# Kernel tuning notes

Hardware: AMD Instinct MI355X
Metric: run time of the kernel (lower is better)

The kernel has to match this reference:

```python
import jax, jax.numpy as jnp
import numpy as np
from jax import lax

B = 32768        # batch
L = 1024         # input_size
K = 5            # kernel_size
PAD = K - 1      # circular padding = 4
FEA = L + (PAD - K // 2) * 2   # mem_fea_dim = 1028
MEM_DIM = 50
DATE_DIM = 32
SHRINK = 0.0025
EPS = 1e-12
DN = ('NCH', 'OIH', 'NCH')


def setup_inputs() -> dict:
    key = jax.random.key(0)
    ks = jax.random.split(key, 10)
    s = 0.05
    return {
        'x': jax.random.normal(ks[0], (B, L), jnp.float32),
        'date_vector': jax.random.normal(ks[1], (B, DATE_DIM), jnp.float32),
        'conv_w': jax.random.normal(ks[2], (1, 1, K), jnp.float32) * s,    # Conv1d weight [out,in,k]
        'convt_w': jax.random.normal(ks[3], (1, 1, K), jnp.float32) * s,   # ConvTranspose1d weight
        'mem_W': jax.random.normal(ks[4], (MEM_DIM, FEA), jnp.float32) * s,      # memory bank (codebook)
        'date_W': jax.random.normal(ks[5], (MEM_DIM, DATE_DIM), jnp.float32) * s, # date addressing weights
        'fcw_w': jax.random.normal(ks[6], (1, L), jnp.float32) * s,
        'fcw_b': jnp.zeros((1,), jnp.float32),
        'fcb_w': jax.random.normal(ks[7], (1, L), jnp.float32) * s,
        'fcb_b': jnp.zeros((1,), jnp.float32),
    }


def _forward(x, date_vector, conv_w, convt_w, mem_W, date_W, fcw_w, fcw_b, fcb_w, fcb_b):
    # --- encode: 1-channel circular conv (bias forced to 0 in original forward) ---
    st = x[:, None, :]                                            # [B,1,L]
    stp = jnp.pad(st, ((0, 0), (0, 0), (PAD, PAD)), mode='wrap')  # circular pad
    st = lax.conv_general_dilated(stp, conv_w, (1,), 'VALID', dimension_numbers=DN)  # [B,1,FEA]

    # --- DateMemoryUnit: date-addressed read with hard shrink + L1 renorm ---
    scores = date_vector @ date_W.T                               # [B,MEM_DIM]
    att = jax.nn.softmax(scores, axis=-1)
    att = jax.nn.relu(att - SHRINK) * att / (jnp.abs(att - SHRINK) + EPS)
    att = att / (jnp.sum(jnp.abs(att), axis=-1, keepdims=True) + EPS)
    st_mem = att @ mem_W                                          # [B,FEA]
    st = st_mem.reshape(B, 1, FEA)

    # --- decode: ConvTranspose1d(k=5, stride=1, padding=4) == VALID conv with flipped kernel ---
    st = lax.conv_general_dilated(st, jnp.flip(convt_w, -1), (1,), 'VALID', dimension_numbers=DN)
    st = st[:, 0, :]                                              # [B,L]

    # --- trend blend ---
    mtf = 0.5
    weight = jnp.tanh(x @ fcw_w.T + fcw_b) * mtf + 1.0            # [B,1]
    bias = jnp.tanh(x @ fcb_w.T + fcb_b) * mtf                    # [B,1]
    st = st * weight + bias
    return st, weight, bias


def reference(x, date_vector, conv_w, convt_w, mem_W, date_W, fcw_w, fcw_b, fcb_w, fcb_b):
    return _forward(x, date_vector, conv_w, convt_w, mem_W, date_W, fcw_w, fcw_b, fcb_w, fcb_b)
```

## Files before the change

kernel.cpp:

```cpp
#include <hip/hip_runtime.h>
#include <hip/hip_bf16.h>

#define BB   32768
#define LL   1024
#define FEA  1028
#define MEM  50
#define DATE 32

typedef float  f32x4  __attribute__((ext_vector_type(4)));
typedef __bf16 bf16x8 __attribute__((ext_vector_type(8)));

__device__ __forceinline__ float wave_max(float v) {
    #pragma unroll
    for (int off = 32; off; off >>= 1) v = fmaxf(v, __shfl_xor(v, off));
    return v;
}
__device__ __forceinline__ float wave_sum(float v) {
    #pragma unroll
    for (int off = 32; off; off >>= 1) v += __shfl_xor(v, off);
    return v;
}

__global__ void prep_wc(const float* __restrict__ convt_w,
                        const float* __restrict__ mem_W,
                        __bf16* __restrict__ wc) {
    int idx = blockIdx.x * 256 + threadIdx.x;
    int n = idx >> 6, k = idx & 63;
    float acc = 0.f;
    if (k < MEM) {
        #pragma unroll
        for (int j = 0; j < 5; ++j)
            acc += convt_w[j] * mem_W[k * FEA + n + 4 - j];
    }
    wc[n * 64 + k] = (__bf16)acc;
}

__global__ __launch_bounds__(256) void memconv_fused(
        const float* __restrict__ x,
        const float* __restrict__ dv,
        const float* __restrict__ dW,
        const float* __restrict__ fcw_w, const float* __restrict__ fcw_b,
        const float* __restrict__ fcb_w, const float* __restrict__ fcb_b,
        const __bf16* __restrict__ wc,
        float* __restrict__ out) {
    __shared__ __bf16 att_s[16 * 80];
    __shared__ float  w_s[16], b_s[16];

    const int lane = threadIdx.x & 63;
    const int wid  = threadIdx.x >> 6;
    const int cg   = lane & 15;
    const int kg   = lane >> 4;
    const int b0   = blockIdx.x * 16;

    {
        int m = lane < MEM ? lane : MEM - 1;
        float dwv[DATE];
        const f32x4* dwp = (const f32x4*)(dW + m * DATE);
        #pragma unroll
        for (int c = 0; c < 8; ++c) {
            f32x4 v = dwp[c];
            #pragma unroll
            for (int j = 0; j < 4; ++j) dwv[c * 4 + j] = v[j];
        }
        #pragma unroll
        for (int rr = 0; rr < 4; ++rr) {
            int r = wid * 4 + rr;
            int b = b0 + r;
            const f32x4* dvp = (const f32x4*)(dv + (size_t)b * DATE);
            float sc = 0.f;
            #pragma unroll
            for (int c = 0; c < 8; ++c) {
                f32x4 v = dvp[c];
                #pragma unroll
                for (int j = 0; j < 4; ++j) sc += v[j] * dwv[c * 4 + j];
            }
            float scm = (lane < MEM) ? sc : -1e30f;
            float mx  = wave_max(scm);
            float e   = (lane < MEM) ? __expf(sc - mx) : 0.f;
            float s   = wave_sum(e);
            float p   = e / s;
            float d   = p - 0.0025f;
            float p2  = (d > 0.f) ? p * d / (d + 1e-12f) : 0.f;
            float s2  = wave_sum(p2) + 1e-12f;
            float att = p2 / s2;
            att_s[r * 80 + lane] = (lane < MEM) ? (__bf16)att : (__bf16)0.f;
        }
    }

    {
        int r = wid * 4 + kg;
        int b = b0 + r;
        float aw = 0.f, ab = 0.f;
        #pragma unroll
        for (int c = 0; c < 16; ++c) {
            int off = c * 64 + cg * 4;
            f32x4 xv = *(const f32x4*)(x + (size_t)b * LL + off);
            f32x4 wv = *(const f32x4*)(fcw_w + off);
            f32x4 bv = *(const f32x4*)(fcb_w + off);
            #pragma unroll
            for (int j = 0; j < 4; ++j) {
                aw += xv[j] * wv[j];
                ab += xv[j] * bv[j];
            }
        }
        #pragma unroll
        for (int off = 1; off <= 8; off <<= 1) {
            aw += __shfl_xor(aw, off);
            ab += __shfl_xor(ab, off);
        }
        if (cg == 0) {
            float w  = tanhf(aw + fcw_b[0]) * 0.5f + 1.0f;
            float bi = tanhf(ab + fcb_b[0]) * 0.5f;
            w_s[r] = w; b_s[r] = bi;
            out[(size_t)BB * LL + b]      = w;
            out[(size_t)BB * LL + BB + b] = bi;
        }
    }
    __syncthreads();

    {
        bf16x8 bfr0 = *(const bf16x8*)(att_s + cg * 80 + kg * 8);
        bf16x8 bfr1 = *(const bf16x8*)(att_s + cg * 80 + 32 + kg * 8);
        float wreg = w_s[cg], breg = b_s[cg];
        float* orow = out + (size_t)(b0 + cg) * LL + wid * 256 + kg * 4;
        const __bf16* wbase = wc + (wid * 256 + cg) * 64 + kg * 8;
        #pragma unroll
        for (int nt = 0; nt < 16; ++nt) {
            bf16x8 a0 = *(const bf16x8*)(wbase + nt * 16 * 64);
            bf16x8 a1 = *(const bf16x8*)(wbase + nt * 16 * 64 + 32);
            f32x4 acc = {0.f, 0.f, 0.f, 0.f};
            acc = __builtin_amdgcn_mfma_f32_16x16x32_bf16(a0, bfr0, acc, 0, 0, 0);
            acc = __builtin_amdgcn_mfma_f32_16x16x32_bf16(a1, bfr1, acc, 0, 0, 0);
            f32x4 v;
            #pragma unroll
            for (int r4 = 0; r4 < 4; ++r4)
                v[r4] = acc[r4] * wreg + breg;
            *(f32x4*)(orow + nt * 16) = v;
        }
    }
}

extern "C" void kernel_launch(void* const* d_in, const int* in_sizes, int n_in,
                              void* d_out, int out_size, void* d_ws, size_t ws_size,
                              hipStream_t stream) {
    const float* x     = (const float*)d_in[0];
    const float* dv    = (const float*)d_in[1];
    const float* convt = (const float*)d_in[3];
    const float* memW  = (const float*)d_in[4];
    const float* dateW = (const float*)d_in[5];
    const float* fcww  = (const float*)d_in[6];
    const float* fcwb  = (const float*)d_in[7];
    const float* fcbw  = (const float*)d_in[8];
    const float* fcbb  = (const float*)d_in[9];
    float* out = (float*)d_out;
    __bf16* wc = (__bf16*)d_ws;

    prep_wc      <<<256,     256, 0, stream>>>(convt, memW, wc);
    memconv_fused<<<BB / 16, 256, 0, stream>>>(x, dv, dateW, fcww, fcwb, fcbw, fcbb, wc, out);
}
```

Before: 285.7 us.

## Stage MFMA output through LDS for coalesced row stores; restructure trend reduction

The MFMA results are written into a per-wave LDS staging tile and then read back so that each store instruction writes 256 contiguous bytes of an output row. Previously each lane wrote 16-byte pieces scattered across 16 rows. The fc trend dot products now read x with full-wave contiguous float4 loads, four rows per wave, and reduce across the whole wave. This adds LDS traffic and about 18KB of shared memory per block, which may lower occupancy.

```diff
diff --git a/kernel.cpp b/kernel.cpp
--- a/kernel.cpp
+++ b/kernel.cpp
@@ -43,8 +43,9 @@
         const float* __restrict__ fcb_w, const float* __restrict__ fcb_b,
         const __bf16* __restrict__ wc,
         float* __restrict__ out) {
-    __shared__ __bf16 att_s[16 * 80];
+    __shared__ __bf16 att_s[16 * 72];
     __shared__ float  w_s[16], b_s[16];
+    __shared__ float  stage[4][16 * 72];
 
     const int lane = threadIdx.x & 63;
     const int wid  = threadIdx.x >> 6;
@@ -65,8 +66,7 @@
         #pragma unroll
         for (int rr = 0; rr < 4; ++rr) {
             int r = wid * 4 + rr;
-            int b = b0 + r;
-            const f32x4* dvp = (const f32x4*)(dv + (size_t)b * DATE);
+            const f32x4* dvp = (const f32x4*)(dv + (size_t)(b0 + r) * DATE);
             float sc = 0.f;
             #pragma unroll
             for (int c = 0; c < 8; ++c) {
@@ -83,59 +83,79 @@
             float p2  = (d > 0.f) ? p * d / (d + 1e-12f) : 0.f;
             float s2  = wave_sum(p2) + 1e-12f;
             float att = p2 / s2;
-            att_s[r * 80 + lane] = (lane < MEM) ? (__bf16)att : (__bf16)0.f;
+            att_s[r * 72 + lane] = (lane < MEM) ? (__bf16)att : (__bf16)0.f;
         }
     }
 
     {
-        int r = wid * 4 + kg;
-        int b = b0 + r;
-        float aw = 0.f, ab = 0.f;
+        f32x4 wv[4], bv[4];
         #pragma unroll
-        for (int c = 0; c < 16; ++c) {
-            int off = c * 64 + cg * 4;
-            f32x4 xv = *(const f32x4*)(x + (size_t)b * LL + off);
-            f32x4 wv = *(const f32x4*)(fcw_w + off);
-            f32x4 bv = *(const f32x4*)(fcb_w + off);
+        for (int c = 0; c < 4; ++c) {
+            wv[c] = *(const f32x4*)(fcw_w + c * 256 + lane * 4);
+            bv[c] = *(const f32x4*)(fcb_w + c * 256 + lane * 4);
+        }
+        f32x4 xv[4][4];
+        #pragma unroll
+        for (int rr = 0; rr < 4; ++rr)
             #pragma unroll
-            for (int j = 0; j < 4; ++j) {
-                aw += xv[j] * wv[j];
-                ab += xv[j] * bv[j];
+            for (int c = 0; c < 4; ++c)
+                xv[rr][c] = *(const f32x4*)(x + (size_t)(b0 + wid * 4 + rr) * LL
+                                              + c * 256 + lane * 4);
+        #pragma unroll
+        for (int rr = 0; rr < 4; ++rr) {
+            int r = wid * 4 + rr;
+            float aw = 0.f, ab = 0.f;
+            #pragma unroll
+            for (int c = 0; c < 4; ++c)
+                #pragma unroll
+                for (int j = 0; j < 4; ++j) {
+                    aw += xv[rr][c][j] * wv[c][j];
+                    ab += xv[rr][c][j] * bv[c][j];
+                }
+            #pragma unroll
+            for (int off = 1; off <= 32; off <<= 1) {
+                aw += __shfl_xor(aw, off);
+                ab += __shfl_xor(ab, off);
             }
-        }
-        #pragma unroll
-        for (int off = 1; off <= 8; off <<= 1) {
-            aw += __shfl_xor(aw, off);
-            ab += __shfl_xor(ab, off);
-        }
-        if (cg == 0) {
             float w  = tanhf(aw + fcw_b[0]) * 0.5f + 1.0f;
             float bi = tanhf(ab + fcb_b[0]) * 0.5f;
-            w_s[r] = w; b_s[r] = bi;
-            out[(size_t)BB * LL + b]      = w;
-            out[(size_t)BB * LL + BB + b] = bi;
+            if (lane == 0) {
+                w_s[r] = w; b_s[r] = bi;
+                out[(size_t)BB * LL + (b0 + r)]      = w;
+                out[(size_t)BB * LL + BB + (b0 + r)] = bi;
+            }
         }
     }
     __syncthreads();
 
     {
-        bf16x8 bfr0 = *(const bf16x8*)(att_s + cg * 80 + kg * 8);
-        bf16x8 bfr1 = *(const bf16x8*)(att_s + cg * 80 + 32 + kg * 8);
-        float wreg = w_s[cg], breg = b_s[cg];
-        float* orow = out + (size_t)(b0 + cg) * LL + wid * 256 + kg * 4;
-        const __bf16* wbase = wc + (wid * 256 + cg) * 64 + kg * 8;
+        bf16x8 bfr0 = *(const bf16x8*)(att_s + cg * 72 + kg * 8);
+        bf16x8 bfr1 = *(const bf16x8*)(att_s + cg * 72 + 32 + kg * 8);
+        float* st = stage[wid];
+        const int n0 = wid * 256;
         #pragma unroll
-        for (int nt = 0; nt < 16; ++nt) {
-            bf16x8 a0 = *(const bf16x8*)(wbase + nt * 16 * 64);
-            bf16x8 a1 = *(const bf16x8*)(wbase + nt * 16 * 64 + 32);
-            f32x4 acc = {0.f, 0.f, 0.f, 0.f};
-            acc = __builtin_amdgcn_mfma_f32_16x16x32_bf16(a0, bfr0, acc, 0, 0, 0);
-            acc = __builtin_amdgcn_mfma_f32_16x16x32_bf16(a1, bfr1, acc, 0, 0, 0);
-            f32x4 v;
+        for (int R = 0; R < 4; ++R) {
             #pragma unroll
-            for (int r4 = 0; r4 < 4; ++r4)
-                v[r4] = acc[r4] * wreg + breg;
-            *(f32x4*)(orow + nt * 16) = v;
+            for (int t = 0; t < 4; ++t) {
+                int n = n0 + (R * 4 + t) * 16 + cg;
+                bf16x8 a0 = *(const bf16x8*)(wc + n * 64 + kg * 8);
+                bf16x8 a1 = *(const bf16x8*)(wc + n * 64 + 32 + kg * 8);
+                f32x4 acc = {0.f, 0.f, 0.f, 0.f};
+                acc = __builtin_amdgcn_mfma_f32_16x16x32_bf16(a0, bfr0, acc, 0, 0, 0);
+                acc = __builtin_amdgcn_mfma_f32_16x16x32_bf16(a1, bfr1, acc, 0, 0, 0);
+                *(f32x4*)(st + cg * 72 + t * 16 + kg * 4) = acc;
+            }
+            #pragma unroll
+            for (int j = 0; j < 4; ++j) {
+                int row = j * 4 + (lane >> 4);
+                int nl  = (lane & 15) * 4;
+                f32x4 v = *(const f32x4*)(st + row * 72 + nl);
+                float w = w_s[row], bi = b_s[row];
+                f32x4 o;
+                #pragma unroll
+                for (int k = 0; k < 4; ++k) o[k] = v[k] * w + bi;
+                *(f32x4*)(out + (size_t)(b0 + row) * LL + n0 + R * 64 + nl) = o;
+            }
         }
     }
 }
```

Measured after the change: 273.7 us. 4.2% less time.
